# Performance work log

Hardware: AMD Instinct MI355X
Metric: run time of the kernel (lower is better)

## Reference

```python
import jax, jax.numpy as jnp
import numpy as np

OUTPUT_SIZE = (7, 7)
SPATIAL_SCALE = 0.25
SAMPLING_RATIO = 2


def setup_inputs() -> dict:
    key = jax.random.key(0)
    k1, k2, k3, k4, k5 = jax.random.split(key, 5)
    N, C, H, W = 2, 256, 200, 304
    R = 1000
    features = jax.random.normal(k1, (N, C, H, W), dtype=jnp.float32)
    # Boxes in IMAGE coordinates (image ~ 800x1216 since spatial_scale=0.25)
    img_h, img_w = H / SPATIAL_SCALE, W / SPATIAL_SCALE
    batch_idx = jax.random.randint(k2, (R,), 0, N).astype(jnp.float32)
    x1 = jax.random.uniform(k3, (R,), minval=0.0, maxval=img_w * 0.8)
    y1 = jax.random.uniform(k4, (R,), minval=0.0, maxval=img_h * 0.8)
    wh = jax.random.uniform(k5, (R, 2), minval=16.0, maxval=256.0)
    x2 = jnp.minimum(x1 + wh[:, 0], img_w - 1.0)
    y2 = jnp.minimum(y1 + wh[:, 1], img_h - 1.0)
    boxes = jnp.stack([batch_idx, x1, y1, x2, y2], axis=1).astype(jnp.float32)
    return {"features": features, "boxes": boxes}


def _axis_interp(coord, size):
    """torchvision bilinear_interpolate clamping along one axis.
    coord: float sample positions. Returns (low_idx, high_idx, frac, valid)."""
    valid = (coord >= -1.0) & (coord <= size)
    c = jnp.maximum(coord, 0.0)
    low_raw = jnp.floor(c).astype(jnp.int32)
    at_edge = low_raw >= size - 1
    low = jnp.where(at_edge, size - 1, low_raw)
    high = jnp.where(at_edge, size - 1, low_raw + 1)
    frac = jnp.where(at_edge, 0.0, c - low_raw.astype(c.dtype))
    return low, high, frac, valid


def roi_align(features, boxes, output_size, spatial_scale, sampling_ratio):
    N, C, H, W = features.shape
    PH, PW = output_size
    G = sampling_ratio
    b = boxes[:, 0].astype(jnp.int32)                      # [R]
    x1 = boxes[:, 1] * spatial_scale
    y1 = boxes[:, 2] * spatial_scale
    x2 = boxes[:, 3] * spatial_scale
    y2 = boxes[:, 4] * spatial_scale
    roi_w = jnp.maximum(x2 - x1, 1.0)
    roi_h = jnp.maximum(y2 - y1, 1.0)
    bin_h = roi_h / PH
    bin_w = roi_w / PW
    off = (jnp.arange(G, dtype=jnp.float32) + 0.5) / G     # [G] sample offsets in bin
    # per-axis sample coords: ys [R,PH,G], xs [R,PW,G]
    ys = y1[:, None, None] + (jnp.arange(PH, dtype=jnp.float32)[None, :, None] + off[None, None, :]) * bin_h[:, None, None]
    xs = x1[:, None, None] + (jnp.arange(PW, dtype=jnp.float32)[None, :, None] + off[None, None, :]) * bin_w[:, None, None]
    yl, yh, fy, vy = _axis_interp(ys, H)
    xl, xh, fx, vx = _axis_interp(xs, W)
    feat = features.transpose(0, 2, 3, 1)                  # [N,H,W,C]
    bb = b[:, None, None, None, None]                      # broadcast to [R,PH,G,PW,G]
    Y = lambda idx: idx[:, :, :, None, None]
    X = lambda idx: idx[:, None, None, :, :]
    # four corner gathers -> [R,PH,G,PW,G,C]
    v_ll = feat[bb, Y(yl), X(xl)]
    v_lh = feat[bb, Y(yl), X(xh)]
    v_hl = feat[bb, Y(yh), X(xl)]
    v_hh = feat[bb, Y(yh), X(xh)]
    fy_b = fy[:, :, :, None, None, None]
    fx_b = fx[:, None, None, :, :, None]
    interp = ((1 - fy_b) * (1 - fx_b) * v_ll + (1 - fy_b) * fx_b * v_lh
              + fy_b * (1 - fx_b) * v_hl + fy_b * fx_b * v_hh)
    valid = (vy[:, :, :, None, None] & vx[:, None, None, :, :])[..., None]
    interp = jnp.where(valid, interp, 0.0)
    pooled = interp.mean(axis=(2, 4))                      # avg over G*G samples -> [R,PH,PW,C]
    return pooled.transpose(0, 3, 1, 2)                    # [R,C,PH,PW]


def reference(features, boxes):
    return roi_align(features, boxes, OUTPUT_SIZE, SPATIAL_SCALE, SAMPLING_RATIO)
```

## Files before the change

### kernel.cpp

```cpp
#include <hip/hip_runtime.h>
#include <hip/hip_bf16.h>


constexpr int N_B  = 2;
constexpr int C_CH = 256;
constexpr int C_HALF = 128;
constexpr int H_F  = 200;
constexpr int W_F  = 304;
constexpr int HW   = H_F * W_F;
constexpr int PH   = 7;
constexpr int PW   = 7;
constexpr int CELLS = PH * PW;
constexpr int CSTRIDE = 56;
constexpr float SCALE = 0.25f;

typedef float  v4f __attribute__((ext_vector_type(4)));

static __device__ __forceinline__ unsigned short f2bf(float f) {
    __hip_bfloat16 h = __float2bfloat16(f);
    return *reinterpret_cast<unsigned short*>(&h);
}
static __device__ __forceinline__ float blo(unsigned int u) {
    return __uint_as_float(u << 16);
}
static __device__ __forceinline__ float bhi(unsigned int u) {
    return __uint_as_float(u & 0xffff0000u);
}

__global__ __launch_bounds__(256) void transpose_nchw_nhwc_bf16(
    const float* __restrict__ in, unsigned short* __restrict__ out)
{
    __shared__ float tile[64][65];
    int tx = blockIdx.x * 64;
    int ty = blockIdx.y * 64;
    int n  = blockIdx.z;
    const float* ip = in  + (size_t)n * C_CH * HW;
    unsigned short* op = out + (size_t)n * HW * C_CH;

    int w4 = threadIdx.x & 15;
    int cr = threadIdx.x >> 4;
#pragma unroll
    for (int p = 0; p < 4; ++p) {
        int c = p * 16 + cr;
        v4f v = __builtin_nontemporal_load(
            (const v4f*)&ip[(size_t)(ty + c) * HW + tx + 4 * w4]);
        tile[c][4 * w4 + 0] = v.x;
        tile[c][4 * w4 + 1] = v.y;
        tile[c][4 * w4 + 2] = v.z;
        tile[c][4 * w4 + 3] = v.w;
    }
    __syncthreads();
    int cq = threadIdx.x & 15;
    int hr = threadIdx.x >> 4;
#pragma unroll
    for (int p = 0; p < 4; ++p) {
        int hw = p * 16 + hr;
        ushort4 v;
        v.x = f2bf(tile[4 * cq + 0][hw]);
        v.y = f2bf(tile[4 * cq + 1][hw]);
        v.z = f2bf(tile[4 * cq + 2][hw]);
        v.w = f2bf(tile[4 * cq + 3][hw]);
        *(ushort4*)&op[(size_t)(tx + hw) * C_CH + ty + 4 * cq] = v;
    }
}

static __device__ __forceinline__ void acc8(
    float* acc, uint4 ll, uint4 lh, uint4 hl, uint4 hh,
    float fxx, float fyy, float w)
{
#define ACC_PAIR(C, I0, I1)                                                   \
    { float a = blo(ll.C), b = blo(lh.C), c = blo(hl.C), d = blo(hh.C);       \
      float lo = a + fxx * (b - a), hi = c + fxx * (d - c);                   \
      acc[I0] += w * (lo + fyy * (hi - lo)); }                                \
    { float a = bhi(ll.C), b = bhi(lh.C), c = bhi(hl.C), d = bhi(hh.C);       \
      float lo = a + fxx * (b - a), hi = c + fxx * (d - c);                   \
      acc[I1] += w * (lo + fyy * (hi - lo)); }
    ACC_PAIR(x, 0, 1)
    ACC_PAIR(y, 2, 3)
    ACC_PAIR(z, 4, 5)
    ACC_PAIR(w, 6, 7)
#undef ACC_PAIR
}

__global__ __launch_bounds__(256) void roi_gather_nhwc(
    const unsigned short* __restrict__ feat_nhwc,
    const float* __restrict__ boxes,
    float* __restrict__ out, int R)
{
    __shared__ alignas(16) float lds[C_HALF * CSTRIDE];
    int r = blockIdx.x;
    if (r >= R) return;
    int chalf = blockIdx.y;
    int tid = threadIdx.x;
    int grp = tid >> 4;
    int ln  = tid & 15;
    int swz = ln & 7;

    const float* box = boxes + r * 5;
    int   b  = (int)box[0];
    float x1 = box[1] * SCALE;
    float y1 = box[2] * SCALE;
    float x2 = box[3] * SCALE;
    float y2 = box[4] * SCALE;
    float bin_w = fmaxf(x2 - x1, 1.0f) * (1.0f / PW);
    float bin_h = fmaxf(y2 - y1, 1.0f) * (1.0f / PH);

    const unsigned short* fb = feat_nhwc + (size_t)b * HW * C_CH
                             + chalf * C_HALF + 8 * ln;

    for (int cell = grp; cell < CELLS; cell += 16) {
        int ph = cell / PW;
        int pw = cell - ph * PW;

        int   yl[2], yh[2]; float fy[2], vy[2];
#pragma unroll
        for (int iy = 0; iy < 2; ++iy) {
            float y = y1 + ((float)ph + (iy ? 0.75f : 0.25f)) * bin_h;
            vy[iy] = (y >= -1.0f && y <= (float)H_F) ? 1.0f : 0.0f;
            float cy = fmaxf(y, 0.0f);
            int ylr = (int)floorf(cy);
            bool e = (ylr >= H_F - 1);
            yl[iy] = e ? H_F - 1 : ylr;
            yh[iy] = e ? H_F - 1 : ylr + 1;
            fy[iy] = e ? 0.0f : cy - (float)ylr;
        }
        int   xl[2], xh[2]; float fx[2], vx[2];
#pragma unroll
        for (int ix = 0; ix < 2; ++ix) {
            float x = x1 + ((float)pw + (ix ? 0.75f : 0.25f)) * bin_w;
            vx[ix] = (x >= -1.0f && x <= (float)W_F) ? 1.0f : 0.0f;
            float cx = fmaxf(x, 0.0f);
            int xlr = (int)floorf(cx);
            bool e = (xlr >= W_F - 1);
            xl[ix] = e ? W_F - 1 : xlr;
            xh[ix] = e ? W_F - 1 : xlr + 1;
            fx[ix] = e ? 0.0f : cx - (float)xlr;
        }

        float acc[8] = {0.f, 0.f, 0.f, 0.f, 0.f, 0.f, 0.f, 0.f};

#pragma unroll
        for (int iy = 0; iy < 2; ++iy) {
            const unsigned short* rl = fb + (size_t)(yl[iy] * W_F) * C_CH;
            const unsigned short* rh = fb + (size_t)(yh[iy] * W_F) * C_CH;
            uint4 l0 = *(const uint4*)(rl + (size_t)xl[0] * C_CH);
            uint4 l1 = *(const uint4*)(rl + (size_t)xh[0] * C_CH);
            uint4 l2 = *(const uint4*)(rl + (size_t)xl[1] * C_CH);
            uint4 l3 = *(const uint4*)(rl + (size_t)xh[1] * C_CH);
            uint4 h0 = *(const uint4*)(rh + (size_t)xl[0] * C_CH);
            uint4 h1 = *(const uint4*)(rh + (size_t)xh[0] * C_CH);
            uint4 h2 = *(const uint4*)(rh + (size_t)xl[1] * C_CH);
            uint4 h3 = *(const uint4*)(rh + (size_t)xh[1] * C_CH);
            acc8(acc, l0, l1, h0, h1, fx[0], fy[iy], vy[iy] * vx[0]);
            acc8(acc, l2, l3, h2, h3, fx[1], fy[iy], vy[iy] * vx[1]);
        }

        int cellx = cell ^ swz;
#pragma unroll
        for (int j = 0; j < 8; ++j)
            lds[(8 * ln + j) * CSTRIDE + cellx] = acc[j] * 0.25f;
    }
    __syncthreads();

    v4f* dst = (v4f*)(out + (size_t)r * (C_CH * CELLS) + chalf * (C_HALF * CELLS));
    for (int q = tid; q < (C_HALF * CELLS) / 4; q += 256) {
        int w0 = 4 * q;
        v4f v;
        {
            int c = w0 / 49, ce = w0 - 49 * c;
            v.x = lds[c * CSTRIDE + (ce ^ ((c >> 3) & 7))];
        }
        {
            int wv = w0 + 1; int c = wv / 49, ce = wv - 49 * c;
            v.y = lds[c * CSTRIDE + (ce ^ ((c >> 3) & 7))];
        }
        {
            int wv = w0 + 2; int c = wv / 49, ce = wv - 49 * c;
            v.z = lds[c * CSTRIDE + (ce ^ ((c >> 3) & 7))];
        }
        {
            int wv = w0 + 3; int c = wv / 49, ce = wv - 49 * c;
            v.w = lds[c * CSTRIDE + (ce ^ ((c >> 3) & 7))];
        }
        __builtin_nontemporal_store(v, dst + q);
    }
}

__global__ __launch_bounds__(256) void roi_align_fallback(
    const float* __restrict__ feat,
    const float* __restrict__ boxes,
    float* __restrict__ out, int total)
{
    int idx = blockIdx.x * 256 + threadIdx.x;
    if (idx >= total) return;
    int pw = idx % PW;
    int t  = idx / PW;
    int ph = t % PH;
    t /= PH;
    int c = t & (C_CH - 1);
    int r = t >> 8;

    const float* box = boxes + r * 5;
    int   b  = (int)box[0];
    float x1 = box[1] * SCALE;
    float y1 = box[2] * SCALE;
    float x2 = box[3] * SCALE;
    float y2 = box[4] * SCALE;
    float bin_w = fmaxf(x2 - x1, 1.0f) * (1.0f / PW);
    float bin_h = fmaxf(y2 - y1, 1.0f) * (1.0f / PH);
    const float* fp = feat + ((size_t)b * C_CH + c) * HW;

    float acc = 0.0f;
#pragma unroll
    for (int iy = 0; iy < 2; ++iy) {
        float y = y1 + ((float)ph + (iy ? 0.75f : 0.25f)) * bin_h;
        bool vy = (y >= -1.0f) && (y <= (float)H_F);
        float cy = fmaxf(y, 0.0f);
        int ylr = (int)floorf(cy);
        int yl, yh; float fyv;
        if (ylr >= H_F - 1) { yl = H_F - 1; yh = H_F - 1; fyv = 0.0f; }
        else                { yl = ylr;     yh = ylr + 1; fyv = cy - (float)ylr; }
#pragma unroll
        for (int ix = 0; ix < 2; ++ix) {
            float x = x1 + ((float)pw + (ix ? 0.75f : 0.25f)) * bin_w;
            bool vx = (x >= -1.0f) && (x <= (float)W_F);
            float cx = fmaxf(x, 0.0f);
            int xlr = (int)floorf(cx);
            int xlv, xhv; float fxv;
            if (xlr >= W_F - 1) { xlv = W_F - 1; xhv = W_F - 1; fxv = 0.0f; }
            else                { xlv = xlr;     xhv = xlr + 1; fxv = cx - (float)xlr; }
            if (vy && vx) {
                const float* rl = fp + yl * W_F;
                const float* rh = fp + yh * W_F;
                float vll = rl[xlv], vlh = rl[xhv], vhl = rh[xlv], vhh = rh[xhv];
                float vlo = vll + fxv * (vlh - vll);
                float vhi = vhl + fxv * (vhh - vhl);
                acc += vlo + fyv * (vhi - vlo);
            }
        }
    }
    out[idx] = acc * 0.25f;
}

extern "C" void kernel_launch(void* const* d_in, const int* in_sizes, int n_in,
                              void* d_out, int out_size, void* d_ws, size_t ws_size,
                              hipStream_t stream) {
    const float* feat  = (const float*)d_in[0];
    const float* boxes = (const float*)d_in[1];
    float* out = (float*)d_out;
    int R = in_sizes[1] / 5;

    size_t need = (size_t)N_B * C_CH * HW * sizeof(unsigned short);
    if (ws_size >= need) {
        unsigned short* nhwc = (unsigned short*)d_ws;
        dim3 tg(HW / 64, C_CH / 64, N_B);
        transpose_nchw_nhwc_bf16<<<tg, 256, 0, stream>>>(feat, nhwc);
        dim3 gg(R, 2);
        roi_gather_nhwc<<<gg, 256, 0, stream>>>(nhwc, boxes, out, R);
    } else {
        int total = out_size;
        roi_align_fallback<<<(total + 255) / 256, 256, 0, stream>>>(feat, boxes, out, total);
    }
}
```

Baseline: 236.6 us.

## Use 512-thread blocks and software-pipeline gather loads across two cells per group

The ROI gather kernel now launches 512 threads per block, so 32 groups cover the 49 cells, each group handling at most two cells. The per-cell loop is unrolled into an explicit schedule that issues the second cell's global loads while the first cell's interpolation math runs. The goal is more memory-level parallelism and latency hiding for the scattered bf16 gathers. In exchange it raises register pressure from holding up to four batches of uint4 loads, and about half the groups sit idle on the second cell.

```diff
diff --git a/kernel.cpp b/kernel.cpp
--- a/kernel.cpp
+++ b/kernel.cpp
@@ -62,6 +62,55 @@
         v.w = f2bf(tile[4 * cq + 3][hw]);
         *(ushort4*)&op[(size_t)(tx + hw) * C_CH + ty + 4 * cq] = v;
     }
+}
+
+struct Geom {
+    int   yl[2], yh[2]; float fy[2], vy[2];
+    int   xl[2], xh[2]; float fx[2], vx[2];
+};
+
+static __device__ __forceinline__ void geom_cell(
+    Geom& g, int cell, float x1, float y1, float bin_w, float bin_h)
+{
+    int ph = cell / PW;
+    int pw = cell - ph * PW;
+#pragma unroll
+    for (int iy = 0; iy < 2; ++iy) {
+        float y = y1 + ((float)ph + (iy ? 0.75f : 0.25f)) * bin_h;
+        g.vy[iy] = (y >= -1.0f && y <= (float)H_F) ? 1.0f : 0.0f;
+        float cy = fmaxf(y, 0.0f);
+        int ylr = (int)floorf(cy);
+        bool e = (ylr >= H_F - 1);
+        g.yl[iy] = e ? H_F - 1 : ylr;
+        g.yh[iy] = e ? H_F - 1 : ylr + 1;
+        g.fy[iy] = e ? 0.0f : cy - (float)ylr;
+    }
+#pragma unroll
+    for (int ix = 0; ix < 2; ++ix) {
+        float x = x1 + ((float)pw + (ix ? 0.75f : 0.25f)) * bin_w;
+        g.vx[ix] = (x >= -1.0f && x <= (float)W_F) ? 1.0f : 0.0f;
+        float cx = fmaxf(x, 0.0f);
+        int xlr = (int)floorf(cx);
+        bool e = (xlr >= W_F - 1);
+        g.xl[ix] = e ? W_F - 1 : xlr;
+        g.xh[ix] = e ? W_F - 1 : xlr + 1;
+        g.fx[ix] = e ? 0.0f : cx - (float)xlr;
+    }
+}
+
+static __device__ __forceinline__ void load_batch(
+    uint4 t[8], const unsigned short* fb, const Geom& g, int iy)
+{
+    const unsigned short* rl = fb + (size_t)(g.yl[iy] * W_F) * C_CH;
+    const unsigned short* rh = fb + (size_t)(g.yh[iy] * W_F) * C_CH;
+    t[0] = *(const uint4*)(rl + (size_t)g.xl[0] * C_CH);
+    t[1] = *(const uint4*)(rl + (size_t)g.xh[0] * C_CH);
+    t[2] = *(const uint4*)(rl + (size_t)g.xl[1] * C_CH);
+    t[3] = *(const uint4*)(rl + (size_t)g.xh[1] * C_CH);
+    t[4] = *(const uint4*)(rh + (size_t)g.xl[0] * C_CH);
+    t[5] = *(const uint4*)(rh + (size_t)g.xh[0] * C_CH);
+    t[6] = *(const uint4*)(rh + (size_t)g.xl[1] * C_CH);
+    t[7] = *(const uint4*)(rh + (size_t)g.xh[1] * C_CH);
 }
 
 static __device__ __forceinline__ void acc8(
@@ -82,7 +131,14 @@
 #undef ACC_PAIR
 }
 
-__global__ __launch_bounds__(256) void roi_gather_nhwc(
+static __device__ __forceinline__ void math_batch(
+    float acc[8], const uint4 t[8], const Geom& g, int iy)
+{
+    acc8(acc, t[0], t[1], t[4], t[5], g.fx[0], g.fy[iy], g.vy[iy] * g.vx[0]);
+    acc8(acc, t[2], t[3], t[6], t[7], g.fx[1], g.fy[iy], g.vy[iy] * g.vx[1]);
+}
+
+__global__ __launch_bounds__(512, 4) void roi_gather_nhwc(
     const unsigned short* __restrict__ feat_nhwc,
     const float* __restrict__ boxes,
     float* __restrict__ out, int R)
@@ -108,62 +164,49 @@
     const unsigned short* fb = feat_nhwc + (size_t)b * HW * C_CH
                              + chalf * C_HALF + 8 * ln;
 
-    for (int cell = grp; cell < CELLS; cell += 16) {
-        int ph = cell / PW;
-        int pw = cell - ph * PW;
-
-        int   yl[2], yh[2]; float fy[2], vy[2];
-#pragma unroll
-        for (int iy = 0; iy < 2; ++iy) {
-            float y = y1 + ((float)ph + (iy ? 0.75f : 0.25f)) * bin_h;
-            vy[iy] = (y >= -1.0f && y <= (float)H_F) ? 1.0f : 0.0f;
-            float cy = fmaxf(y, 0.0f);
-            int ylr = (int)floorf(cy);
-            bool e = (ylr >= H_F - 1);
-            yl[iy] = e ? H_F - 1 : ylr;
-            yh[iy] = e ? H_F - 1 : ylr + 1;
-            fy[iy] = e ? 0.0f : cy - (float)ylr;
-        }
-        int   xl[2], xh[2]; float fx[2], vx[2];
-#pragma unroll
-        for (int ix = 0; ix < 2; ++ix) {
-            float x = x1 + ((float)pw + (ix ? 0.75f : 0.25f)) * bin_w;
-            vx[ix] = (x >= -1.0f && x <= (float)W_F) ? 1.0f : 0.0f;
-            float cx = fmaxf(x, 0.0f);
-            int xlr = (int)floorf(cx);
-            bool e = (xlr >= W_F - 1);
-            xl[ix] = e ? W_F - 1 : xlr;
-            xh[ix] = e ? W_F - 1 : xlr + 1;
-            fx[ix] = e ? 0.0f : cx - (float)xlr;
-        }
-
-        float acc[8] = {0.f, 0.f, 0.f, 0.f, 0.f, 0.f, 0.f, 0.f};
-
-#pragma unroll
-        for (int iy = 0; iy < 2; ++iy) {
-            const unsigned short* rl = fb + (size_t)(yl[iy] * W_F) * C_CH;
-            const unsigned short* rh = fb + (size_t)(yh[iy] * W_F) * C_CH;
-            uint4 l0 = *(const uint4*)(rl + (size_t)xl[0] * C_CH);
-            uint4 l1 = *(const uint4*)(rl + (size_t)xh[0] * C_CH);
-            uint4 l2 = *(const uint4*)(rl + (size_t)xl[1] * C_CH);
-            uint4 l3 = *(const uint4*)(rl + (size_t)xh[1] * C_CH);
-            uint4 h0 = *(const uint4*)(rh + (size_t)xl[0] * C_CH);
-            uint4 h1 = *(const uint4*)(rh + (size_t)xh[0] * C_CH);
-            uint4 h2 = *(const uint4*)(rh + (size_t)xl[1] * C_CH);
-            uint4 h3 = *(const uint4*)(rh + (size_t)xh[1] * C_CH);
-            acc8(acc, l0, l1, h0, h1, fx[0], fy[iy], vy[iy] * vx[0]);
-            acc8(acc, l2, l3, h2, h3, fx[1], fy[iy], vy[iy] * vx[1]);
-        }
-
-        int cellx = cell ^ swz;
+    int cellA = grp;
+    int cellB = grp + 32;
+    bool hasB = (cellB < CELLS);
+
+    Geom gA, gB;
+    geom_cell(gA, cellA, x1, y1, bin_w, bin_h);
+    if (hasB) geom_cell(gB, cellB, x1, y1, bin_w, bin_h);
+
+    uint4 a0[8], a1[8];
+    load_batch(a0, fb, gA, 0);
+    load_batch(a1, fb, gA, 1);
+
+    float accA[8] = {0.f, 0.f, 0.f, 0.f, 0.f, 0.f, 0.f, 0.f};
+    math_batch(accA, a0, gA, 0);
+
+    uint4 b0[8];
+    if (hasB) load_batch(b0, fb, gB, 0);
+
+    math_batch(accA, a1, gA, 1);
+
+    uint4 b1[8];
+    if (hasB) load_batch(b1, fb, gB, 1);
+
+    {
+        int cellx = cellA ^ swz;
 #pragma unroll
         for (int j = 0; j < 8; ++j)
-            lds[(8 * ln + j) * CSTRIDE + cellx] = acc[j] * 0.25f;
+            lds[(8 * ln + j) * CSTRIDE + cellx] = accA[j] * 0.25f;
+    }
+
+    if (hasB) {
+        float accB[8] = {0.f, 0.f, 0.f, 0.f, 0.f, 0.f, 0.f, 0.f};
+        math_batch(accB, b0, gB, 0);
+        math_batch(accB, b1, gB, 1);
+        int cellx = cellB ^ swz;
+#pragma unroll
+        for (int j = 0; j < 8; ++j)
+            lds[(8 * ln + j) * CSTRIDE + cellx] = accB[j] * 0.25f;
     }
     __syncthreads();
 
     v4f* dst = (v4f*)(out + (size_t)r * (C_CH * CELLS) + chalf * (C_HALF * CELLS));
-    for (int q = tid; q < (C_HALF * CELLS) / 4; q += 256) {
+    for (int q = tid; q < (C_HALF * CELLS) / 4; q += 512) {
         int w0 = 4 * q;
         v4f v;
         {
@@ -256,7 +299,7 @@
         dim3 tg(HW / 64, C_CH / 64, N_B);
         transpose_nchw_nhwc_bf16<<<tg, 256, 0, stream>>>(feat, nhwc);
         dim3 gg(R, 2);
-        roi_gather_nhwc<<<gg, 256, 0, stream>>>(nhwc, boxes, out, R);
+        roi_gather_nhwc<<<gg, 512, 0, stream>>>(nhwc, boxes, out, R);
     } else {
         int total = out_size;
         roi_align_fallback<<<(total + 255) / 256, 256, 0, stream>>>(feat, boxes, out, total);
```

Measured after the change: 270.6 us. +14.4%, slower.
